# Optimization experiments

Measured on AMD Instinct MI355X. Metric: run time of the kernel, lower is better.

## Reference

```python
import jax, jax.numpy as jnp
import numpy as np

N_HEAD = 16
D_HEAD = 64
D_MODEL = 1024  # d_qry = d_key = d_val
D_HIDDEN = N_HEAD * D_HEAD


def setup_inputs() -> dict:
    key = jax.random.key(0)
    ks = jax.random.split(key, 9)
    b, n = 2, 2048
    s = 0.02
    return {
        "qry": jax.random.normal(ks[0], (b, n, D_MODEL), jnp.float32),
        "key": jax.random.normal(ks[1], (b, n, D_MODEL), jnp.float32),
        "val": jax.random.normal(ks[2], (b, n, D_MODEL), jnp.float32),
        "mask": jax.random.randint(ks[3], (b, n), 0, 2) > 0,  # key-side padding mask
        "Wq": jax.random.normal(ks[4], (D_MODEL, D_HIDDEN), jnp.float32) * s,
        "Wk": jax.random.normal(ks[5], (D_MODEL, D_HIDDEN), jnp.float32) * s,
        "Wv": jax.random.normal(ks[6], (D_MODEL, D_HIDDEN), jnp.float32) * s,
        "Wo": jax.random.normal(ks[7], (D_HIDDEN, D_MODEL), jnp.float32) * s,
        "bo": jax.random.normal(ks[8], (D_MODEL,), jnp.float32) * s,
    }


def reference(qry, key, val, mask, Wq, Wk, Wv, Wo, bo):
    b, n, _ = qry.shape
    scale = D_HEAD ** 0.5
    # projections, split into heads: [b, h, n, d]
    q = (qry @ Wq).reshape(b, n, N_HEAD, D_HEAD).transpose(0, 2, 1, 3)
    k = (key @ Wk).reshape(b, n, N_HEAD, D_HEAD).transpose(0, 2, 1, 3)
    v = (val @ Wv).reshape(b, n, N_HEAD, D_HEAD).transpose(0, 2, 1, 3)
    sim = jnp.einsum('bhid,bhjd->bhij', q, k) / scale  # full O(n^2) scores
    # key-side padding mask broadcast over heads and query positions
    sim = jnp.where(mask[:, None, None, :], sim, jnp.float32(-1e32))
    attn = jax.nn.softmax(sim, axis=-1)
    # NOTE: original applies dropout to `sim` after computing attn (a no-op on
    # the output); dropout=0.0 regardless, so attention weights are `attn`.
    x = jnp.einsum('bhij,bhjd->bhid', attn, v)
    x = x.transpose(0, 2, 1, 3).reshape(b, n, D_HIDDEN)
    return x @ Wo + bo
```

## Files before the change

### kernel.cpp

```cpp
#include <hip/hip_runtime.h>
#include <hip/hip_bf16.h>

using u16 = unsigned short;
using u32 = unsigned int;
using short8 = __attribute__((ext_vector_type(8))) short;
using f32x4  = __attribute__((ext_vector_type(4))) float;
using u32x4  = __attribute__((ext_vector_type(4))) u32;
using u32x2  = __attribute__((ext_vector_type(2))) u32;

union V16 { u32x4 u; short8 s; };

__device__ __forceinline__ u16 f2b(float f) {
  u32 u = __float_as_uint(f);
  u32 r = (u + 0x7FFFu + ((u >> 16) & 1u)) >> 16;
  return (u16)r;
}
__device__ __forceinline__ u32 pk2(u16 a, u16 b) {
  return (u32)a | ((u32)b << 16);
}
__device__ __forceinline__ u32 cvtpk(float lo, float hi) {
  u32 r;
  asm("v_cvt_pk_bf16_f32 %0, %1, %2" : "=v"(r) : "v"(lo), "v"(hi));
  return r;
}
__device__ __forceinline__ float ex2(float x) {
  float r;
  asm("v_exp_f32 %0, %1" : "=v"(r) : "v"(x));
  return r;
}
__device__ __forceinline__ void gld16(const u16* g, u16* l) {
  __builtin_amdgcn_global_load_lds(
      (const __attribute__((address_space(1))) u32*)g,
      (__attribute__((address_space(3))) u32*)l, 16, 0, 0);
}

#define KSCALE 0.18033688011f
#define SMAX   12.0f


__global__ __launch_bounds__(256) void wconv(
    const float* __restrict__ Wq, const float* __restrict__ Wk,
    const float* __restrict__ Wv, const float* __restrict__ Wo,
    u16* __restrict__ Wt, u16* __restrict__ WoT)
{
  __shared__ u16 T[64][130];
  const int zz = blockIdx.z;
  const float* src = (zz == 0) ? Wq : (zz == 1) ? Wk : (zz == 2) ? Wv : Wo;
  u16* dst = (zz < 3) ? (Wt + (size_t)zz * 1048576) : WoT;
  const int nt = blockIdx.x, ks = blockIdx.y;
  const int tid = threadIdx.x;

  {
    const int kl = tid >> 2, nl0 = (tid & 3) * 32;
    const float* sp = src + (size_t)(ks * 64 + kl) * 1024 + nt * 128 + nl0;
#pragma unroll
    for (int i = 0; i < 8; ++i) {
      f32x4 x = *(const f32x4*)(sp + i * 4);
      T[kl][nl0 + i * 4 + 0] = f2b(x[0]);
      T[kl][nl0 + i * 4 + 1] = f2b(x[1]);
      T[kl][nl0 + i * 4 + 2] = f2b(x[2]);
      T[kl][nl0 + i * 4 + 3] = f2b(x[3]);
    }
  }
  __syncthreads();

  const int c = tid >> 4, l0 = (tid & 15) * 4;
  u16* dp = dst + ((size_t)(nt * 16 + ks) * 16 + c) * 512 + l0 * 8;
#pragma unroll
  for (int dl = 0; dl < 4; ++dl) {
    const int l = l0 + dl;
    const int kl = (c & 1) * 32 + (l >> 4) * 8;
    const int nl = (c >> 3) * 64 + ((c >> 1) & 3) * 16 + (l & 15);
    u32x4 u;
#pragma unroll
    for (int p = 0; p < 4; ++p)
      u[p] = pk2(T[kl + 2 * p][nl], T[kl + 2 * p + 1][nl]);
    *(u32x4*)(dp + dl * 8) = u;
  }
}

__global__ __launch_bounds__(256) void aconv(
    const float* __restrict__ Aq, const float* __restrict__ Ak,
    const float* __restrict__ Av, u16* __restrict__ Af,
    int z0, size_t zstride)
{
  const int z = blockIdx.z + z0;
  const float* A = (z == 0) ? Aq : (z == 1) ? Ak : Av;
  u16* dst = Af + (size_t)blockIdx.z * zstride;
  const int ks = blockIdx.x, mt = blockIdx.y;
  const int tid = threadIdx.x;
  const int r = tid >> 1, h = tid & 1;

  const f32x4* sp = (const f32x4*)(A + (size_t)(mt * 128 + r) * 1024 + ks * 64 + h * 32);
  const int c = ((r >> 6) << 3) | (((r >> 4) & 3) << 1) | h;
  u16* dp = dst + ((size_t)(mt * 16 + ks) * 16 + c) * 512 + (r & 15) * 8;

#pragma unroll
  for (int lg = 0; lg < 4; ++lg) {
    f32x4 x0 = sp[2 * lg], x1 = sp[2 * lg + 1];
    u32x4 u;
    u[0] = cvtpk(x0[0], x0[1]); u[1] = cvtpk(x0[2], x0[3]);
    u[2] = cvtpk(x1[0], x1[1]); u[3] = cvtpk(x1[2], x1[3]);
    *(u32x4*)(dp + lg * 128) = u;
  }
}

__global__ __launch_bounds__(256) void maskscan(
    const int* __restrict__ mask, int* __restrict__ cidx,
    float* __restrict__ cbias, int* __restrict__ ntb,
    u16* __restrict__ Kimg, u16* __restrict__ Vimg)
{
  const int h = blockIdx.x, b = blockIdx.y;
  const int tid = threadIdx.x;
  __shared__ int ssum[256];

  int m8[8], s = 0;
#pragma unroll
  for (int i = 0; i < 8; ++i) {
    m8[i] = mask[b * 2048 + tid * 8 + i] ? 1 : 0;
    s += m8[i];
  }
  ssum[tid] = s;
  __syncthreads();
  for (int off = 1; off < 256; off <<= 1) {
    int v = (tid >= off) ? ssum[tid - off] : 0;
    __syncthreads();
    ssum[tid] += v;
    __syncthreads();
  }
  const int nvalid = ssum[255];
  int run = ssum[tid] - s;

  if (h == 0) {
#pragma unroll
    for (int i = 0; i < 8; ++i) {
      cidx[b * 2048 + tid * 8 + i] = m8[i] ? run : -1;
      run += m8[i];
    }
#pragma unroll
    for (int i = 0; i < 8; ++i) {
      const int idx = tid * 8 + i;
      cbias[b * 2048 + idx] = (idx < nvalid) ? -SMAX : -1e30f;
    }
    if (tid == 0) ntb[b] = (nvalid + 63) >> 6;
  }

  const int pend = ((nvalid + 63) >> 6) << 6;
  for (int p = nvalid + tid; p < pend; p += 256) {
    const int kt2 = p >> 6, r = p & 63;
    const size_t base = ((size_t)((b * 16 + h) * 32 + kt2)) * 4096;
    const int t2 = ((r >> 5) << 1) | ((r >> 2) & 1);
    const int ll2 = (((r >> 3) & 3) << 2) | (r & 3);
#pragma unroll
    for (int s2 = 0; s2 < 2; ++s2)
#pragma unroll
      for (int lgk = 0; lgk < 4; ++lgk)
#pragma unroll
        for (int e = 0; e < 8; ++e)
          Kimg[base + (t2 * 2 + s2) * 512 + (lgk * 16 + ll2) * 8 + e] = 0;
    const int sv = r >> 5, lgv = (r >> 3) & 3, e0 = r & 7;
#pragma unroll
    for (int td = 0; td < 4; ++td)
#pragma unroll
      for (int llv = 0; llv < 16; ++llv)
        Vimg[base + (sv * 4 + td) * 512 + (lgv * 16 + llv) * 8 + e0] = 0;
  }
}

__global__ __launch_bounds__(512, 4) void gemm_qkv_k(
    const u16* __restrict__ Af, const u16* __restrict__ Wt,
    u16* __restrict__ Qw, u16* __restrict__ Kw, u16* __restrict__ Vw,
    const int* __restrict__ cidx, int z0, size_t azs)
{
  __shared__ u16 As[2][8192];
  __shared__ u16 Bs[2][8192];

  const int L = blockIdx.x;
  const int xcd = L & 7, idx = L >> 3;
  const int mt = (xcd << 2) | (idx & 3);
  const int nt = (idx >> 2) & 7;
  const int zi = idx >> 5;
  const int z = z0 + zi;

  const u16* Aimg = Af + (size_t)zi * azs;
  const u16* Bimg = Wt + (size_t)z * 1048576;
  u16* O = (z == 0) ? Qw : (z == 1) ? Kw : Vw;

  const int tid = threadIdx.x;
  const int w = tid >> 6, l = tid & 63, lg = l >> 4, ll = l & 15;
  const int wr = w >> 2, wc = w & 3;
  const size_t ab = (size_t)mt * 131072;
  const size_t bb = (size_t)nt * 131072;

  f32x4 acc[4][2];
#pragma unroll
  for (int i = 0; i < 4; ++i)
#pragma unroll
    for (int t = 0; t < 2; ++t)
      acc[i][t] = (f32x4){0.f, 0.f, 0.f, 0.f};

#define QKV_ISSUE(ksx, buf) do {                                           \
    const size_t ao_ = ab + (size_t)(ksx) * 8192;                          \
    const size_t bo_ = bb + (size_t)(ksx) * 8192;                          \
    gld16(Aimg + ao_ + (size_t)w * 512 + l * 8,       &As[buf][w * 512]);  \
    gld16(Aimg + ao_ + (size_t)(w + 8) * 512 + l * 8, &As[buf][(w + 8) * 512]); \
    gld16(Bimg + bo_ + (size_t)w * 512 + l * 8,       &Bs[buf][w * 512]);  \
    gld16(Bimg + bo_ + (size_t)(w + 8) * 512 + l * 8, &Bs[buf][(w + 8) * 512]); \
  } while (0)

  QKV_ISSUE(0, 0);

  for (int ks = 0; ks < 16; ++ks) {
    const int cur = ks & 1;
    asm volatile("s_waitcnt vmcnt(0)" ::: "memory");
    __builtin_amdgcn_sched_barrier(0);
    __builtin_amdgcn_s_barrier();
    __builtin_amdgcn_sched_barrier(0);

    if (ks + 1 < 16) QKV_ISSUE(ks + 1, cur ^ 1);

    short8 afr[2][4], bfr[2][2];
#pragma unroll
    for (int kk = 0; kk < 2; ++kk) {
#pragma unroll
      for (int i = 0; i < 4; ++i) {
        V16 v; v.u = *(const u32x4*)&As[cur][(wr * 8 + i * 2 + kk) * 512 + l * 8];
        afr[kk][i] = v.s;
      }
#pragma unroll
      for (int t = 0; t < 2; ++t) {
        V16 v; v.u = *(const u32x4*)&Bs[cur][((wc >> 1) * 8 + ((wc & 1) * 2 + t) * 2 + kk) * 512 + l * 8];
        bfr[kk][t] = v.s;
      }
    }
#pragma unroll
    for (int kk = 0; kk < 2; ++kk)
#pragma unroll
      for (int i = 0; i < 4; ++i)
#pragma unroll
        for (int t = 0; t < 2; ++t)
          acc[i][t] = __builtin_amdgcn_mfma_f32_16x16x32_bf16(afr[kk][i], bfr[kk][t], acc[i][t], 0, 0, 0);
  }
#undef QKV_ISSUE

  const int m0 = mt * 128, n0 = nt * 128;
  if (z == 0) {
#pragma unroll
    for (int i = 0; i < 4; ++i)
#pragma unroll
      for (int t = 0; t < 2; ++t) {
        const int n = n0 + wc * 32 + t * 16 + ll;
        const int h = n >> 6, dd = n & 63;
#pragma unroll
        for (int j = 0; j < 4; ++j) {
          const int m = m0 + wr * 64 + i * 16 + lg * 4 + j;
          const int bbk = m >> 11, pos = m & 2047;
          O[((size_t)(bbk * 16 + h) * 2048 + pos) * 64 + dd] = f2b(acc[i][t][j]);
        }
      }
  } else if (z == 1) {
#pragma unroll
    for (int i = 0; i < 4; ++i)
#pragma unroll
      for (int t = 0; t < 2; ++t) {
        const int n = n0 + wc * 32 + t * 16 + ll;
        const int h = n >> 6, dd = n & 63;
        const int s = dd >> 5, lgk = (dd >> 3) & 3, e = dd & 7;
        const int m_ = m0 + wr * 64 + i * 16 + lg * 4;
        const int bbk = m_ >> 11, pos0 = m_ & 2047;
        const int4 cp = *(const int4*)&cidx[bbk * 2048 + pos0];
        const int cpa[4] = {cp.x, cp.y, cp.z, cp.w};
#pragma unroll
        for (int j = 0; j < 4; ++j) {
          const int pp = cpa[j];
          if (pp >= 0) {
            const int kt2 = pp >> 6, r = pp & 63;
            const int t2 = ((r >> 5) << 1) | ((r >> 2) & 1);
            const int ll2 = (((r >> 3) & 3) << 2) | (r & 3);
            O[((size_t)((bbk * 16 + h) * 32 + kt2)) * 4096 + (t2 * 2 + s) * 512 + (lgk * 16 + ll2) * 8 + e]
                = f2b(acc[i][t][j] * KSCALE);
          }
        }
      }
  } else {
#pragma unroll
    for (int i = 0; i < 4; ++i)
#pragma unroll
      for (int t = 0; t < 2; ++t) {
        const int n = n0 + wc * 32 + t * 16 + ll;
        const int h = n >> 6, dd = n & 63;
        const int td = dd >> 4, llv = dd & 15;
        const int m_ = m0 + wr * 64 + i * 16 + lg * 4;
        const int bbk = m_ >> 11, pos0 = m_ & 2047;
        const int4 cp = *(const int4*)&cidx[bbk * 2048 + pos0];
        const int cpa[4] = {cp.x, cp.y, cp.z, cp.w};
#pragma unroll
        for (int j = 0; j < 4; ++j) {
          const int pp = cpa[j];
          if (pp >= 0) {
            const int kt2 = pp >> 6, kk = pp & 63;
            const int s = kk >> 5, lgv = (kk >> 3) & 3, e0 = kk & 7;
            O[((size_t)((bbk * 16 + h) * 32 + kt2)) * 4096 + (s * 4 + td) * 512 + (lgv * 16 + llv) * 8 + e0]
                = f2b(acc[i][t][j]);
          }
        }
      }
  }
}

__global__ __launch_bounds__(256) void attn_k(
    const u16* __restrict__ Q, const u16* __restrict__ Kt, const u16* __restrict__ Vt,
    const float* __restrict__ cbias, const int* __restrict__ ntb,
    u16* __restrict__ Xf)
{
  __shared__ u16 Ls[2][8192];

  const int tid = threadIdx.x;
  const int w = tid >> 6, l = tid & 63, lg = l >> 4, ll = l & 15;
  const int qb = blockIdx.x, h = blockIdx.y, b = blockIdx.z;
  const size_t qbase = (size_t)(b * 16 + h) * 2048 * 64;
  const size_t tbase = (size_t)((b * 16 + h) * 32) * 4096;
  const int q0 = qb * 128 + w * 32;
  const int ntiles = ntb[b];

  short8 aq[2][2];
#pragma unroll
  for (int g = 0; g < 2; ++g)
#pragma unroll
    for (int s = 0; s < 2; ++s) {
      V16 v; v.u = *(const u32x4*)&Q[qbase + (size_t)(q0 + g * 16 + ll) * 64 + s * 32 + lg * 8];
      aq[g][s] = v.s;
    }

  float lrow[2] = {0.f, 0.f};
  f32x4 o[2][4];
#pragma unroll
  for (int g = 0; g < 2; ++g)
#pragma unroll
    for (int td = 0; td < 4; ++td) o[g][td] = (f32x4){0.f, 0.f, 0.f, 0.f};

  u32x4 rg[4];
#pragma unroll
  for (int q = 0; q < 4; ++q) {
    const int c = w * 4 + q;
    const u16* src = (c < 8) ? Kt : Vt;
    rg[q] = *(const u32x4*)&src[tbase + (c & 7) * 512 + l * 8];
  }
#pragma unroll
  for (int q = 0; q < 4; ++q)
    *(u32x4*)&Ls[0][(w * 4 + q) * 512 + l * 8] = rg[q];
  if (ntiles > 1) {
#pragma unroll
    for (int q = 0; q < 4; ++q) {
      const int c = w * 4 + q;
      const u16* src = (c < 8) ? Kt : Vt;
      rg[q] = *(const u32x4*)&src[tbase + 4096 + (c & 7) * 512 + l * 8];
    }
  }
  asm volatile("s_waitcnt lgkmcnt(0)" ::: "memory");
  __builtin_amdgcn_sched_barrier(0);
  __builtin_amdgcn_s_barrier();
  __builtin_amdgcn_sched_barrier(0);

  for (int kt = 0; kt < ntiles; ++kt) {
    const int cur = kt & 1;
    const int j0 = kt * 64;
    const u16* Lc = Ls[cur];

    f32x4 sc[2][4];
    __builtin_amdgcn_s_setprio(1);
#pragma unroll
    for (int t = 0; t < 4; ++t) {
      short8 bk0, bk1;
      { V16 v; v.u = *(const u32x4*)&Lc[(t * 2 + 0) * 512 + l * 8]; bk0 = v.s; }
      { V16 v; v.u = *(const u32x4*)&Lc[(t * 2 + 1) * 512 + l * 8]; bk1 = v.s; }
      f32x4 a0 = (f32x4){0.f, 0.f, 0.f, 0.f};
      f32x4 a1 = (f32x4){0.f, 0.f, 0.f, 0.f};
      a0 = __builtin_amdgcn_mfma_f32_16x16x32_bf16(bk0, aq[0][0], a0, 0, 0, 0);
      a1 = __builtin_amdgcn_mfma_f32_16x16x32_bf16(bk0, aq[1][0], a1, 0, 0, 0);
      a0 = __builtin_amdgcn_mfma_f32_16x16x32_bf16(bk1, aq[0][1], a0, 0, 0, 0);
      a1 = __builtin_amdgcn_mfma_f32_16x16x32_bf16(bk1, aq[1][1], a1, 0, 0, 0);
      const f32x4 cb = *(const f32x4*)&cbias[b * 2048 + j0 + ((t >> 1) << 5) + ((t & 1) << 2) + (lg << 3)];
#pragma unroll
      for (int j = 0; j < 4; ++j) {
        sc[0][t][j] = a0[j] + cb[j];
        sc[1][t][j] = a1[j] + cb[j];
      }
    }
    __builtin_amdgcn_s_setprio(0);

#pragma unroll
    for (int g = 0; g < 2; ++g) {
      f32x4 s4 = (f32x4){0.f, 0.f, 0.f, 0.f};
#pragma unroll
      for (int t = 0; t < 4; ++t)
#pragma unroll
        for (int j = 0; j < 4; ++j) {
          sc[g][t][j] = ex2(sc[g][t][j]);
          s4[j] += sc[g][t][j];
        }
      float rs = (s4[0] + s4[1]) + (s4[2] + s4[3]);
      rs += __shfl_xor(rs, 16);
      rs += __shfl_xor(rs, 32);
      lrow[g] += rs;
    }

    __builtin_amdgcn_s_setprio(1);
#pragma unroll
    for (int s = 0; s < 2; ++s) {
      V16 pb0, pb1;
      pb0.u[0] = cvtpk(sc[0][2 * s][0], sc[0][2 * s][1]);
      pb0.u[1] = cvtpk(sc[0][2 * s][2], sc[0][2 * s][3]);
      pb0.u[2] = cvtpk(sc[0][2 * s + 1][0], sc[0][2 * s + 1][1]);
      pb0.u[3] = cvtpk(sc[0][2 * s + 1][2], sc[0][2 * s + 1][3]);
      pb1.u[0] = cvtpk(sc[1][2 * s][0], sc[1][2 * s][1]);
      pb1.u[1] = cvtpk(sc[1][2 * s][2], sc[1][2 * s][3]);
      pb1.u[2] = cvtpk(sc[1][2 * s + 1][0], sc[1][2 * s + 1][1]);
      pb1.u[3] = cvtpk(sc[1][2 * s + 1][2], sc[1][2 * s + 1][3]);
#pragma unroll
      for (int td = 0; td < 4; ++td) {
        V16 v; v.u = *(const u32x4*)&Lc[4096 + (s * 4 + td) * 512 + l * 8];
        o[0][td] = __builtin_amdgcn_mfma_f32_16x16x32_bf16(v.s, pb0.s, o[0][td], 0, 0, 0);
        o[1][td] = __builtin_amdgcn_mfma_f32_16x16x32_bf16(v.s, pb1.s, o[1][td], 0, 0, 0);
      }
    }
    __builtin_amdgcn_s_setprio(0);

    if (kt + 1 < ntiles) {
#pragma unroll
      for (int q = 0; q < 4; ++q)
        *(u32x4*)&Ls[cur ^ 1][(w * 4 + q) * 512 + l * 8] = rg[q];
    }
    if (kt + 2 < ntiles) {
#pragma unroll
      for (int q = 0; q < 4; ++q) {
        const int c = w * 4 + q;
        const u16* src = (c < 8) ? Kt : Vt;
        rg[q] = *(const u32x4*)&src[tbase + (size_t)(kt + 2) * 4096 + (c & 7) * 512 + l * 8];
      }
    }
    asm volatile("s_waitcnt lgkmcnt(0)" ::: "memory");
    __builtin_amdgcn_sched_barrier(0);
    __builtin_amdgcn_s_barrier();
    __builtin_amdgcn_sched_barrier(0);
  }

#pragma unroll
  for (int g = 0; g < 2; ++g) {
    const float inv = 1.f / lrow[g];
    const int m = b * 2048 + q0 + g * 16 + ll;
    const int mt = m >> 7, mr = m & 127;
    const int e0 = (lg & 1) * 4;
#pragma unroll
    for (int td = 0; td < 4; ++td) {
      const int c = ((mr >> 6) << 3) | (((mr >> 4) & 3) << 1) | (td >> 1);
      const int lA = (((td << 1) + (lg >> 1)) & 3) * 16 + (mr & 15);
      u32x2 wv;
      wv[0] = cvtpk(o[g][td][0] * inv, o[g][td][1] * inv);
      wv[1] = cvtpk(o[g][td][2] * inv, o[g][td][3] * inv);
      *(u32x2*)&Xf[((size_t)(mt * 16 + h) * 16 + c) * 512 + lA * 8 + e0] = wv;
    }
  }
}

__global__ __launch_bounds__(512, 4) void gemm_out_k(
    const u16* __restrict__ Xf, const u16* __restrict__ WoF,
    const float* __restrict__ bo, float* __restrict__ out)
{
  __shared__ u16 As[3][8192];
  __shared__ u16 Bs[3][8192];

  const int L = blockIdx.x;
  const int xcd = L & 7, idx = L >> 3;
  const int mt = (xcd << 2) | (idx & 3);
  const int nt = idx >> 2;

  const int tid = threadIdx.x;
  const int w = tid >> 6, l = tid & 63, lg = l >> 4, ll = l & 15;
  const int wr = w >> 2, wc = w & 3;
  const size_t ab = (size_t)mt * 131072;
  const size_t bb = (size_t)nt * 131072;

  f32x4 acc[4][2];
#pragma unroll
  for (int i = 0; i < 4; ++i)
#pragma unroll
    for (int t = 0; t < 2; ++t)
      acc[i][t] = (f32x4){0.f, 0.f, 0.f, 0.f};

#define OUT_ISSUE(ksx, buf) do {                                           \
    const size_t ao_ = ab + (size_t)(ksx) * 8192;                          \
    const size_t bo_ = bb + (size_t)(ksx) * 8192;                          \
    gld16(Xf + ao_ + (size_t)w * 512 + l * 8,        &As[buf][w * 512]);   \
    gld16(Xf + ao_ + (size_t)(w + 8) * 512 + l * 8,  &As[buf][(w + 8) * 512]); \
    gld16(WoF + bo_ + (size_t)w * 512 + l * 8,       &Bs[buf][w * 512]);   \
    gld16(WoF + bo_ + (size_t)(w + 8) * 512 + l * 8, &Bs[buf][(w + 8) * 512]); \
  } while (0)

  OUT_ISSUE(0, 0);
  OUT_ISSUE(1, 1);

  for (int ks = 0; ks < 16; ++ks) {
    const int cur = ks % 3;
    if (ks < 15) asm volatile("s_waitcnt vmcnt(4)" ::: "memory");
    else         asm volatile("s_waitcnt vmcnt(0)" ::: "memory");
    __builtin_amdgcn_sched_barrier(0);
    __builtin_amdgcn_s_barrier();
    __builtin_amdgcn_sched_barrier(0);

    if (ks + 2 < 16) OUT_ISSUE(ks + 2, (ks + 2) % 3);

    short8 afr[2][4], bfr[2][2];
#pragma unroll
    for (int kk = 0; kk < 2; ++kk) {
#pragma unroll
      for (int i = 0; i < 4; ++i) {
        V16 v; v.u = *(const u32x4*)&As[cur][(wr * 8 + i * 2 + kk) * 512 + l * 8];
        afr[kk][i] = v.s;
      }
#pragma unroll
      for (int t = 0; t < 2; ++t) {
        V16 v; v.u = *(const u32x4*)&Bs[cur][((wc >> 1) * 8 + ((wc & 1) * 2 + t) * 2 + kk) * 512 + l * 8];
        bfr[kk][t] = v.s;
      }
    }
#pragma unroll
    for (int kk = 0; kk < 2; ++kk)
#pragma unroll
      for (int i = 0; i < 4; ++i)
#pragma unroll
        for (int t = 0; t < 2; ++t)
          acc[i][t] = __builtin_amdgcn_mfma_f32_16x16x32_bf16(afr[kk][i], bfr[kk][t], acc[i][t], 0, 0, 0);
  }
#undef OUT_ISSUE

  const int m0 = mt * 128, n0 = nt * 128;
#pragma unroll
  for (int i = 0; i < 4; ++i)
#pragma unroll
    for (int t = 0; t < 2; ++t) {
      const int n = n0 + wc * 32 + t * 16 + ll;
      const float bv = bo[n];
#pragma unroll
      for (int j = 0; j < 4; ++j) {
        const int m = m0 + wr * 64 + i * 16 + lg * 4 + j;
        out[(size_t)m * 1024 + n] = acc[i][t][j] + bv;
      }
    }
}

extern "C" void kernel_launch(void* const* d_in, const int* in_sizes, int n_in,
                              void* d_out, int out_size, void* d_ws, size_t ws_size,
                              hipStream_t stream) {
  const float* qry = (const float*)d_in[0];
  const float* key = (const float*)d_in[1];
  const float* val = (const float*)d_in[2];
  const int* mask  = (const int*)d_in[3];
  const float* Wq  = (const float*)d_in[4];
  const float* Wk  = (const float*)d_in[5];
  const float* Wv  = (const float*)d_in[6];
  const float* Wo  = (const float*)d_in[7];
  const float* bo  = (const float*)d_in[8];
  float* out = (float*)d_out;

  char* ws = (char*)d_ws;
  u16* Wt  = (u16*)(ws);
  u16* WoT = (u16*)(ws + 6291456);
  u16* Qw  = (u16*)(ws + 8388608);
  u16* Kw  = (u16*)(ws + 16777216);
  u16* Vw  = (u16*)(ws + 25165824);
  u16* Af  = (u16*)(ws + 33554432);
  u16* Xw  = (u16*)(ws + 33554432);

  int*   cidx  = (int*)d_out;
  float* cbias = (float*)((char*)d_out + 16384);
  int*   ntb   = (int*)((char*)d_out + 32768);

  wconv<<<dim3(8, 16, 4), 256, 0, stream>>>(Wq, Wk, Wv, Wo, Wt, WoT);
  maskscan<<<dim3(16, 2), 256, 0, stream>>>(mask, cidx, cbias, ntb, Kw, Vw);

  const bool big = (ws_size >= 58720256ull);
  if (big) {
    aconv<<<dim3(16, 32, 3), 256, 0, stream>>>(qry, key, val, Af, 0, 4194304);
    gemm_qkv_k<<<dim3(768, 1, 1), 512, 0, stream>>>(Af, Wt, Qw, Kw, Vw, cidx, 0, 4194304);
  } else {
    for (int z = 0; z < 3; ++z) {
      aconv<<<dim3(16, 32, 1), 256, 0, stream>>>(qry, key, val, Af, z, 0);
      gemm_qkv_k<<<dim3(256, 1, 1), 512, 0, stream>>>(Af, Wt, Qw, Kw, Vw, cidx, z, 0);
    }
  }
  attn_k<<<dim3(16, 16, 2), 256, 0, stream>>>(Qw, Kw, Vw, cbias, ntb, Xw);
  gemm_out_k<<<dim3(256, 1, 1), 512, 0, stream>>>(Xw, WoT, bo, out);
}
```

Measured before the change: 107.4 us.

## Compact valid key/value rows before projection GEMM and skip padded tiles

Result: no change. 106.3 us (-1.0%).

```diff
diff --git a/kernel.cpp b/kernel.cpp
--- a/kernel.cpp
+++ b/kernel.cpp
@@ -79,9 +79,72 @@
   }
 }
 
+__global__ __launch_bounds__(256) void maskscan(
+    const int* __restrict__ mask, int* __restrict__ inv,
+    float* __restrict__ cbias, int* __restrict__ ntb,
+    u16* __restrict__ Kimg, u16* __restrict__ Vimg)
+{
+  const int h = blockIdx.x, b = blockIdx.y;
+  const int tid = threadIdx.x;
+  __shared__ int ssum[256];
+
+  int m8[8], s = 0;
+#pragma unroll
+  for (int i = 0; i < 8; ++i) {
+    m8[i] = mask[b * 2048 + tid * 8 + i] ? 1 : 0;
+    s += m8[i];
+  }
+  ssum[tid] = s;
+  __syncthreads();
+  for (int off = 1; off < 256; off <<= 1) {
+    int v = (tid >= off) ? ssum[tid - off] : 0;
+    __syncthreads();
+    ssum[tid] += v;
+    __syncthreads();
+  }
+  const int nvalid = ssum[255];
+  int run = ssum[tid] - s;
+
+  if (h == 0) {
+    int run2 = run;
+#pragma unroll
+    for (int i = 0; i < 8; ++i) {
+      if (m8[i]) { inv[b * 2048 + run2] = tid * 8 + i; ++run2; }
+    }
+#pragma unroll
+    for (int i = 0; i < 8; ++i) {
+      const int idx = tid * 8 + i;
+      cbias[b * 2048 + idx] = (idx < nvalid) ? -SMAX : -1e30f;
+    }
+    if (tid == 0) { ntb[b] = (nvalid + 63) >> 6; ntb[2 + b] = nvalid; }
+  }
+
+  const int pend = ((nvalid + 63) >> 6) << 6;
+  for (int p = nvalid + tid; p < pend; p += 256) {
+    const int kt2 = p >> 6, r = p & 63;
+    const size_t base = ((size_t)((b * 16 + h) * 32 + kt2)) * 4096;
+    const int t2 = ((r >> 5) << 1) | ((r >> 2) & 1);
+    const int ll2 = (((r >> 3) & 3) << 2) | (r & 3);
+#pragma unroll
+    for (int s2 = 0; s2 < 2; ++s2)
+#pragma unroll
+      for (int lgk = 0; lgk < 4; ++lgk)
+#pragma unroll
+        for (int e = 0; e < 8; ++e)
+          Kimg[base + (t2 * 2 + s2) * 512 + (lgk * 16 + ll2) * 8 + e] = 0;
+    const int sv = r >> 5, lgv = (r >> 3) & 3, e0 = r & 7;
+#pragma unroll
+    for (int td = 0; td < 4; ++td)
+#pragma unroll
+      for (int llv = 0; llv < 16; ++llv)
+        Vimg[base + (sv * 4 + td) * 512 + (lgv * 16 + llv) * 8 + e0] = 0;
+  }
+}
+
 __global__ __launch_bounds__(256) void aconv(
     const float* __restrict__ Aq, const float* __restrict__ Ak,
     const float* __restrict__ Av, u16* __restrict__ Af,
+    const int* __restrict__ inv, const int* __restrict__ ntbv,
     int z0, size_t zstride)
 {
   const int z = blockIdx.z + z0;
@@ -91,7 +154,14 @@
   const int tid = threadIdx.x;
   const int r = tid >> 1, h = tid & 1;
 
-  const f32x4* sp = (const f32x4*)(A + (size_t)(mt * 128 + r) * 1024 + ks * 64 + h * 32);
+  int srow = mt * 128 + r;
+  if (z >= 1) {
+    const int b = srow >> 11, cpos = srow & 2047;
+    if (cpos >= ntbv[2 + b]) return;
+    srow = b * 2048 + inv[b * 2048 + cpos];
+  }
+
+  const f32x4* sp = (const f32x4*)(A + (size_t)srow * 1024 + ks * 64 + h * 32);
   const int c = ((r >> 6) << 3) | (((r >> 4) & 3) << 1) | h;
   u16* dp = dst + ((size_t)(mt * 16 + ks) * 16 + c) * 512 + (r & 15) * 8;
 
@@ -105,72 +175,10 @@
   }
 }
 
-__global__ __launch_bounds__(256) void maskscan(
-    const int* __restrict__ mask, int* __restrict__ cidx,
-    float* __restrict__ cbias, int* __restrict__ ntb,
-    u16* __restrict__ Kimg, u16* __restrict__ Vimg)
-{
-  const int h = blockIdx.x, b = blockIdx.y;
-  const int tid = threadIdx.x;
-  __shared__ int ssum[256];
-
-  int m8[8], s = 0;
-#pragma unroll
-  for (int i = 0; i < 8; ++i) {
-    m8[i] = mask[b * 2048 + tid * 8 + i] ? 1 : 0;
-    s += m8[i];
-  }
-  ssum[tid] = s;
-  __syncthreads();
-  for (int off = 1; off < 256; off <<= 1) {
-    int v = (tid >= off) ? ssum[tid - off] : 0;
-    __syncthreads();
-    ssum[tid] += v;
-    __syncthreads();
-  }
-  const int nvalid = ssum[255];
-  int run = ssum[tid] - s;
-
-  if (h == 0) {
-#pragma unroll
-    for (int i = 0; i < 8; ++i) {
-      cidx[b * 2048 + tid * 8 + i] = m8[i] ? run : -1;
-      run += m8[i];
-    }
-#pragma unroll
-    for (int i = 0; i < 8; ++i) {
-      const int idx = tid * 8 + i;
-      cbias[b * 2048 + idx] = (idx < nvalid) ? -SMAX : -1e30f;
-    }
-    if (tid == 0) ntb[b] = (nvalid + 63) >> 6;
-  }
-
-  const int pend = ((nvalid + 63) >> 6) << 6;
-  for (int p = nvalid + tid; p < pend; p += 256) {
-    const int kt2 = p >> 6, r = p & 63;
-    const size_t base = ((size_t)((b * 16 + h) * 32 + kt2)) * 4096;
-    const int t2 = ((r >> 5) << 1) | ((r >> 2) & 1);
-    const int ll2 = (((r >> 3) & 3) << 2) | (r & 3);
-#pragma unroll
-    for (int s2 = 0; s2 < 2; ++s2)
-#pragma unroll
-      for (int lgk = 0; lgk < 4; ++lgk)
-#pragma unroll
-        for (int e = 0; e < 8; ++e)
-          Kimg[base + (t2 * 2 + s2) * 512 + (lgk * 16 + ll2) * 8 + e] = 0;
-    const int sv = r >> 5, lgv = (r >> 3) & 3, e0 = r & 7;
-#pragma unroll
-    for (int td = 0; td < 4; ++td)
-#pragma unroll
-      for (int llv = 0; llv < 16; ++llv)
-        Vimg[base + (sv * 4 + td) * 512 + (lgv * 16 + llv) * 8 + e0] = 0;
-  }
-}
-
 __global__ __launch_bounds__(512, 4) void gemm_qkv_k(
     const u16* __restrict__ Af, const u16* __restrict__ Wt,
     u16* __restrict__ Qw, u16* __restrict__ Kw, u16* __restrict__ Vw,
-    const int* __restrict__ cidx, int z0, size_t azs)
+    const int* __restrict__ ntbv, int z0, size_t azs)
 {
   __shared__ u16 As[2][8192];
   __shared__ u16 Bs[2][8192];
@@ -181,6 +189,11 @@
   const int nt = (idx >> 2) & 7;
   const int zi = idx >> 5;
   const int z = z0 + zi;
+
+  if (z >= 1) {
+    const int b0 = (mt * 128) >> 11;
+    if ((mt * 128 & 2047) >= ntbv[2 + b0]) return;
+  }
 
   const u16* Aimg = Af + (size_t)zi * azs;
   const u16* Bimg = Wt + (size_t)z * 1048576;
@@ -259,6 +272,8 @@
         }
       }
   } else if (z == 1) {
+    const int bbk = m0 >> 11;
+    const int nv = ntbv[2 + bbk];
 #pragma unroll
     for (int i = 0; i < 4; ++i)
 #pragma unroll
@@ -266,15 +281,12 @@
         const int n = n0 + wc * 32 + t * 16 + ll;
         const int h = n >> 6, dd = n & 63;
         const int s = dd >> 5, lgk = (dd >> 3) & 3, e = dd & 7;
-        const int m_ = m0 + wr * 64 + i * 16 + lg * 4;
-        const int bbk = m_ >> 11, pos0 = m_ & 2047;
-        const int4 cp = *(const int4*)&cidx[bbk * 2048 + pos0];
-        const int cpa[4] = {cp.x, cp.y, cp.z, cp.w};
 #pragma unroll
         for (int j = 0; j < 4; ++j) {
-          const int pp = cpa[j];
-          if (pp >= 0) {
-            const int kt2 = pp >> 6, r = pp & 63;
+          const int m = m0 + wr * 64 + i * 16 + lg * 4 + j;
+          const int cpos = m & 2047;
+          if (cpos < nv) {
+            const int kt2 = cpos >> 6, r = cpos & 63;
             const int t2 = ((r >> 5) << 1) | ((r >> 2) & 1);
             const int ll2 = (((r >> 3) & 3) << 2) | (r & 3);
             O[((size_t)((bbk * 16 + h) * 32 + kt2)) * 4096 + (t2 * 2 + s) * 512 + (lgk * 16 + ll2) * 8 + e]
@@ -283,6 +295,8 @@
         }
       }
   } else {
+    const int bbk = m0 >> 11;
+    const int nv = ntbv[2 + bbk];
 #pragma unroll
     for (int i = 0; i < 4; ++i)
 #pragma unroll
@@ -290,19 +304,20 @@
         const int n = n0 + wc * 32 + t * 16 + ll;
         const int h = n >> 6, dd = n & 63;
         const int td = dd >> 4, llv = dd & 15;
-        const int m_ = m0 + wr * 64 + i * 16 + lg * 4;
-        const int bbk = m_ >> 11, pos0 = m_ & 2047;
-        const int4 cp = *(const int4*)&cidx[bbk * 2048 + pos0];
-        const int cpa[4] = {cp.x, cp.y, cp.z, cp.w};
-#pragma unroll
-        for (int j = 0; j < 4; ++j) {
-          const int pp = cpa[j];
-          if (pp >= 0) {
-            const int kt2 = pp >> 6, kk = pp & 63;
-            const int s = kk >> 5, lgv = (kk >> 3) & 3, e0 = kk & 7;
-            O[((size_t)((bbk * 16 + h) * 32 + kt2)) * 4096 + (s * 4 + td) * 512 + (lgv * 16 + llv) * 8 + e0]
-                = f2b(acc[i][t][j]);
-          }
+        const int mb0 = m0 + wr * 64 + i * 16 + lg * 4;
+        const int cp0 = mb0 & 2047;
+        const int kt2 = cp0 >> 6, kk = cp0 & 63;
+        const int s = kk >> 5, lgv = (kk >> 3) & 3, e0 = kk & 7;
+        u16* dstp = &O[((size_t)((bbk * 16 + h) * 32 + kt2)) * 4096 + (s * 4 + td) * 512 + (lgv * 16 + llv) * 8 + e0];
+        if (cp0 + 3 < nv) {
+          u32x2 wv;
+          wv[0] = pk2(f2b(acc[i][t][0]), f2b(acc[i][t][1]));
+          wv[1] = pk2(f2b(acc[i][t][2]), f2b(acc[i][t][3]));
+          *(u32x2*)dstp = wv;
+        } else {
+#pragma unroll
+          for (int j = 0; j < 4; ++j)
+            if (cp0 + j < nv) dstp[j] = f2b(acc[i][t][j]);
         }
       }
   }
@@ -447,7 +462,7 @@
 
 #pragma unroll
   for (int g = 0; g < 2; ++g) {
-    const float inv = 1.f / lrow[g];
+    const float inv2 = 1.f / lrow[g];
     const int m = b * 2048 + q0 + g * 16 + ll;
     const int mt = m >> 7, mr = m & 127;
     const int e0 = (lg & 1) * 4;
@@ -456,8 +471,8 @@
       const int c = ((mr >> 6) << 3) | (((mr >> 4) & 3) << 1) | (td >> 1);
       const int lA = (((td << 1) + (lg >> 1)) & 3) * 16 + (mr & 15);
       u32x2 wv;
-      wv[0] = cvtpk(o[g][td][0] * inv, o[g][td][1] * inv);
-      wv[1] = cvtpk(o[g][td][2] * inv, o[g][td][3] * inv);
+      wv[0] = cvtpk(o[g][td][0] * inv2, o[g][td][1] * inv2);
+      wv[1] = cvtpk(o[g][td][2] * inv2, o[g][td][3] * inv2);
       *(u32x2*)&Xf[((size_t)(mt * 16 + h) * 16 + c) * 512 + lA * 8 + e0] = wv;
     }
   }
@@ -572,21 +587,21 @@
   u16* Af  = (u16*)(ws + 33554432);
   u16* Xw  = (u16*)(ws + 33554432);
 
-  int*   cidx  = (int*)d_out;
+  int*   inv   = (int*)d_out;
   float* cbias = (float*)((char*)d_out + 16384);
   int*   ntb   = (int*)((char*)d_out + 32768);
 
   wconv<<<dim3(8, 16, 4), 256, 0, stream>>>(Wq, Wk, Wv, Wo, Wt, WoT);
-  maskscan<<<dim3(16, 2), 256, 0, stream>>>(mask, cidx, cbias, ntb, Kw, Vw);
+  maskscan<<<dim3(16, 2), 256, 0, stream>>>(mask, inv, cbias, ntb, Kw, Vw);
 
   const bool big = (ws_size >= 58720256ull);
   if (big) {
-    aconv<<<dim3(16, 32, 3), 256, 0, stream>>>(qry, key, val, Af, 0, 4194304);
-    gemm_qkv_k<<<dim3(768, 1, 1), 512, 0, stream>>>(Af, Wt, Qw, Kw, Vw, cidx, 0, 4194304);
+    aconv<<<dim3(16, 32, 3), 256, 0, stream>>>(qry, key, val, Af, inv, ntb, 0, 4194304);
+    gemm_qkv_k<<<dim3(768, 1, 1), 512, 0, stream>>>(Af, Wt, Qw, Kw, Vw, ntb, 0, 4194304);
   } else {
     for (int z = 0; z < 3; ++z) {
-      aconv<<<dim3(16, 32, 1), 256, 0, stream>>>(qry, key, val, Af, z, 0);
-      gemm_qkv_k<<<dim3(256, 1, 1), 512, 0, stream>>>(Af, Wt, Qw, Kw, Vw, cidx, z, 0);
+      aconv<<<dim3(16, 32, 1), 256, 0, stream>>>(qry, key, val, Af, inv, ntb, z, 0);
+      gemm_qkv_k<<<dim3(256, 1, 1), 512, 0, stream>>>(Af, Wt, Qw, Kw, Vw, ntb, z, 0);
     }
   }
   attn_k<<<dim3(16, 16, 2), 256, 0, stream>>>(Qw, Kw, Vw, cbias, ntb, Xw);
```
